# Kernel optimization log

Hardware: AMD Instinct MI355X
Metric: run time of the kernel (lower is better)

The kernel has to match this reference:

```python
import jax, jax.numpy as jnp
import numpy as np

EPS = 1e-5
GROUPS = 32


def group_norm(x, gamma, beta):
    # x: [b, c, h, w]
    b, c, h, w = x.shape
    xg = x.reshape(b, GROUPS, c // GROUPS, h, w)
    mu = jnp.mean(xg, axis=(2, 3, 4), keepdims=True)
    var = jnp.var(xg, axis=(2, 3, 4), keepdims=True)
    xg = (xg - mu) / jnp.sqrt(var + EPS)
    x = xg.reshape(b, c, h, w)
    return x * gamma[None, :, None, None] + beta[None, :, None, None]


def conv1x1(x, w, bias):
    # x: [b, c_in, h, w], w: [c_out, c_in] -> [b, c_out, h, w]
    return jnp.einsum('oc,bchw->bohw', w, x) + bias[None, :, None, None]


def setup_inputs() -> dict:
    key = jax.random.key(0)
    ks = jax.random.split(key, 6)
    c = 512
    s = 1.0 / np.sqrt(c)
    x = jax.random.normal(ks[0], (8, c, 64, 64), dtype=jnp.float32)
    return {
        'x': x,
        'gn_gamma': jnp.ones((c,), jnp.float32),
        'gn_beta': jnp.zeros((c,), jnp.float32),
        'wq': jax.random.normal(ks[1], (c, c), jnp.float32) * s,
        'bq': jnp.zeros((c,), jnp.float32),
        'wk': jax.random.normal(ks[2], (c, c), jnp.float32) * s,
        'bk': jnp.zeros((c,), jnp.float32),
        'wv': jax.random.normal(ks[3], (c, c), jnp.float32) * s,
        'bv': jnp.zeros((c,), jnp.float32),
        'wo': jax.random.normal(ks[4], (c, c), jnp.float32) * s,
        'bo': jnp.zeros((c,), jnp.float32),
    }


def reference(x, gn_gamma, gn_beta, wq, bq, wk, bk, wv, bv, wo, bo):
    b, c, h, w = x.shape
    hidden = group_norm(x, gn_gamma, gn_beta)
    q = conv1x1(hidden, wq, bq).reshape(b, c, h * w).transpose(0, 2, 1)  # [b, hw, c]
    k = conv1x1(hidden, wk, bk).reshape(b, c, h * w)                      # [b, c, hw]
    v = conv1x1(hidden, wv, bv).reshape(b, c, h * w).transpose(0, 2, 1)  # [b, hw, c]
    # NOTE: faithful to source — attention logits are MULTIPLIED by sqrt(c)
    attn = jnp.einsum('bqc,bck->bqk', q, k) * jnp.float32(c) ** 0.5
    attn = jax.nn.softmax(attn, axis=-1)
    attn_h = jnp.einsum('bqk,bkc->bqc', attn, v)                          # [b, hw, c]
    attn_h = attn_h.transpose(0, 2, 1).reshape(b, c, h, w)
    return x + conv1x1(attn_h, wo, bo)
```

## Files before the change

### kernel.cpp

```cpp
#include <hip/hip_runtime.h>
#include <stdint.h>

typedef unsigned short u16;
typedef unsigned int u32;
typedef __attribute__((ext_vector_type(4))) float f32x4;
typedef __attribute__((ext_vector_type(8))) __bf16 bf16x8;
typedef __attribute__((ext_vector_type(4))) unsigned short u16x4;

#define DEVINL __device__ __forceinline__

DEVINL u16 f2bf(float f) {
  u32 u = __builtin_bit_cast(u32, f);
  u32 r = (u + 0x7fffu + ((u >> 16) & 1u)) >> 16;
  return (u16)r;
}
DEVINL float bf2f(u16 h) {
  u32 u = ((u32)h) << 16;
  return __builtin_bit_cast(float, u);
}

DEVINL f32x4 mfma16(bf16x8 a, bf16x8 b, f32x4 c) {
  return __builtin_amdgcn_mfma_f32_16x16x32_bf16(a, b, c, 0, 0, 0);
}

DEVINL void gload_lds16(const void* g, void* l) {
  auto gp = (__attribute__((address_space(1))) void*)(reinterpret_cast<uintptr_t>(g));
  auto lp = (__attribute__((address_space(3))) void*)(u32)(reinterpret_cast<uintptr_t>(l));
  __builtin_amdgcn_global_load_lds(gp, lp, 16, 0, 0);
}

template <int ROWS, int KCS, int NT>
DEVINL void stage_tile(const u16* __restrict__ g, int ld, char* lds, int tid) {
  constexpr int SWZ = (KCS - 1) < 7 ? (KCS - 1) : 7;
  constexpr int CH = ROWS * KCS;
#pragma unroll
  for (int c0 = 0; c0 < CH; c0 += NT) {
    int c = c0 + tid;
    int row = c / KCS;
    int slot = c & (KCS - 1);
    const u16* src = g + (size_t)row * ld + ((slot ^ (row & SWZ)) << 3);
    char* dst = lds + (((size_t)(c0 + (tid & ~63))) << 4);
    gload_lds16(src, dst);
  }
}

template <int KCS, int SWZM>
DEVINL bf16x8 fragk(const char* lds, int row, int kslot) {
  return *reinterpret_cast<const bf16x8*>(
      lds + (size_t)row * (KCS * 16) + (size_t)((kslot ^ (row & SWZM)) << 4));
}

__global__ __launch_bounds__(256) void gn_stats(const float* __restrict__ x,
                                                float* __restrict__ smean,
                                                float* __restrict__ srstd) {
  const int bg = blockIdx.x;
  const float4* base = reinterpret_cast<const float4*>(x + (size_t)bg * 65536);
  float s = 0.f, ss = 0.f;
  for (int i = threadIdx.x; i < 16384; i += 256) {
    float4 v = base[i];
    s += v.x + v.y + v.z + v.w;
    ss += v.x * v.x + v.y * v.y + v.z * v.z + v.w * v.w;
  }
#pragma unroll
  for (int off = 1; off < 64; off <<= 1) {
    s += __shfl_xor(s, off);
    ss += __shfl_xor(ss, off);
  }
  __shared__ float rs_[4], rss_[4];
  int w = threadIdx.x >> 6;
  if ((threadIdx.x & 63) == 0) { rs_[w] = s; rss_[w] = ss; }
  __syncthreads();
  if (threadIdx.x == 0) {
    float S = rs_[0] + rs_[1] + rs_[2] + rs_[3];
    float SS = rss_[0] + rss_[1] + rss_[2] + rss_[3];
    float mu = S * (1.0f / 65536.0f);
    float var = SS * (1.0f / 65536.0f) - mu * mu;
    smean[bg] = mu;
    srstd[bg] = 1.0f / sqrtf(var + 1e-5f);
  }
}

__global__ __launch_bounds__(256) void gn_apply(
    const float* __restrict__ x, const float* __restrict__ gamma,
    const float* __restrict__ beta, const float* __restrict__ smean,
    const float* __restrict__ srstd, u16* __restrict__ hhi, u16* __restrict__ hlo) {
  __shared__ __align__(16) u16 thi[128][136];
  __shared__ __align__(16) u16 tlo[128][136];
  const int b = blockIdx.z, p0 = blockIdx.y * 128, c0 = blockIdx.x * 128;
  const int tid = threadIdx.x;
  const int ci = tid >> 1, ph = tid & 1;
  const int c = c0 + ci;
  const int bg = b * 32 + (c >> 4);
  const float mu = smean[bg], rstd = srstd[bg];
  const float ga = gamma[c] * rstd;
  const float be = beta[c] - mu * ga;
  const float* xrow = x + ((size_t)(b * 512 + c)) * 4096 + p0;
#pragma unroll
  for (int s = 0; s < 16; s++) {
    int pj = ph * 4 + s * 8;
    float4 v = *reinterpret_cast<const float4*>(xrow + pj);
    float h0 = v.x * ga + be, h1 = v.y * ga + be, h2 = v.z * ga + be, h3 = v.w * ga + be;
    u16 a0 = f2bf(h0), a1 = f2bf(h1), a2 = f2bf(h2), a3 = f2bf(h3);
    thi[pj + 0][ci] = a0; tlo[pj + 0][ci] = f2bf(h0 - bf2f(a0));
    thi[pj + 1][ci] = a1; tlo[pj + 1][ci] = f2bf(h1 - bf2f(a1));
    thi[pj + 2][ci] = a2; tlo[pj + 2][ci] = f2bf(h2 - bf2f(a2));
    thi[pj + 3][ci] = a3; tlo[pj + 3][ci] = f2bf(h3 - bf2f(a3));
  }
  __syncthreads();
  u16* oh = hhi + ((size_t)b * 4096 + p0) * 512 + c0;
  u16* ol = hlo + ((size_t)b * 4096 + p0) * 512 + c0;
  for (int cc = tid; cc < 2048; cc += 256) {
    int p = cc >> 4, sli = cc & 15;
    *reinterpret_cast<bf16x8*>(oh + (size_t)p * 512 + sli * 8) =
        *reinterpret_cast<const bf16x8*>(&thi[p][sli * 8]);
    *reinterpret_cast<bf16x8*>(ol + (size_t)p * 512 + sli * 8) =
        *reinterpret_cast<const bf16x8*>(&tlo[p][sli * 8]);
  }
}

__global__ __launch_bounds__(256) void prep_w(
    const float* __restrict__ wq, const float* __restrict__ wk,
    const float* __restrict__ wv, const float* __restrict__ wo,
    u16* __restrict__ wqh, u16* __restrict__ wql, u16* __restrict__ wkh,
    u16* __restrict__ wkl, u16* __restrict__ wvb, u16* __restrict__ wob) {
  int i = blockIdx.x * 256 + threadIdx.x;
  if (i >= 262144) return;
  float a = wq[i]; u16 h = f2bf(a); wqh[i] = h; wql[i] = f2bf(a - bf2f(h));
  float bb = wk[i]; h = f2bf(bb); wkh[i] = h; wkl[i] = f2bf(bb - bf2f(h));
  wvb[i] = f2bf(wv[i]);
  wob[i] = f2bf(wo[i]);
}

template <int MODE>
__global__ __launch_bounds__(256, 2) void conv_gemm(
    const u16* __restrict__ A0, const u16* __restrict__ A1,
    const u16* __restrict__ B0, const u16* __restrict__ B1,
    const float* __restrict__ bias, const float* __restrict__ xres,
    u16* __restrict__ o0, u16* __restrict__ o1, float* __restrict__ of,
    long sAb, long sBb) {
  constexpr int LDSZ = (MODE == 0) ? 65536 : ((MODE == 1) ? 34816 : 32768);
  __shared__ __align__(16) char lds[LDSZ];
  char* ldsA = lds;
  char* ldsB = lds + 16384;

  const int b = blockIdx.z;
  const int n0 = blockIdx.x * 128;
  const int m0 = blockIdx.y * 128;
  const int tid = threadIdx.x;
  const int lane = tid & 63;
  const int w = tid >> 6;
  const int li = lane & 15, gq = lane >> 4;
  const int wm = (w >> 1) * 64, wn = (w & 1) * 64;

  const u16* Ag = A0 + (size_t)b * sAb + (size_t)m0 * 512;
  const u16* Bg = B0 + (size_t)b * sBb + (size_t)n0 * 512;
  const u16* Ag1 = (MODE == 0) ? (A1 + (size_t)b * sAb + (size_t)m0 * 512) : nullptr;
  const u16* Bg1 = (MODE == 0) ? (B1 + (size_t)b * sBb + (size_t)n0 * 512) : nullptr;

  f32x4 acc[4][4] = {};

  for (int k0 = 0; k0 < 512; k0 += 64) {
    __syncthreads();
    stage_tile<128, 8, 256>(Ag + k0, 512, ldsA, tid);
    stage_tile<128, 8, 256>(Bg + k0, 512, ldsB, tid);
    if (MODE == 0) {
      stage_tile<128, 8, 256>(Ag1 + k0, 512, lds + 32768, tid);
      stage_tile<128, 8, 256>(Bg1 + k0, 512, lds + 49152, tid);
    }
    __syncthreads();
#pragma unroll
    for (int kk = 0; kk < 2; kk++) {
      bf16x8 aF[4], bF[4], aL[4], bL[4];
#pragma unroll
      for (int t = 0; t < 4; t++) {
        aF[t] = fragk<8, 7>(ldsA, wm + t * 16 + li, kk * 4 + gq);
        bF[t] = fragk<8, 7>(ldsB, wn + t * 16 + li, kk * 4 + gq);
        if (MODE == 0) {
          aL[t] = fragk<8, 7>(lds + 32768, wm + t * 16 + li, kk * 4 + gq);
          bL[t] = fragk<8, 7>(lds + 49152, wn + t * 16 + li, kk * 4 + gq);
        }
      }
#pragma unroll
      for (int mt = 0; mt < 4; mt++)
#pragma unroll
        for (int nt = 0; nt < 4; nt++) {
          acc[mt][nt] = mfma16(aF[mt], bF[nt], acc[mt][nt]);
          if (MODE == 0) {
            acc[mt][nt] = mfma16(aF[mt], bL[nt], acc[mt][nt]);
            acc[mt][nt] = mfma16(aL[mt], bF[nt], acc[mt][nt]);
          }
        }
    }
  }

  if (MODE == 0) {
#pragma unroll
    for (int nt = 0; nt < 4; nt++) {
      int gn = n0 + wn + nt * 16 + li;
      float bs = bias[gn];
#pragma unroll
      for (int mt = 0; mt < 4; mt++)
#pragma unroll
        for (int r = 0; r < 4; r++) {
          int gm = m0 + wm + mt * 16 + gq * 4 + r;
          float v = acc[mt][nt][r] + bs;
          u16 hi = f2bf(v);
          size_t idx = ((size_t)b * 4096 + gm) * 512 + gn;
          o0[idx] = hi;
          o1[idx] = f2bf(v - bf2f(hi));
        }
    }
  } else if (MODE == 1) {
    __syncthreads();
    u16* vt = (u16*)lds;
#pragma unroll
    for (int nt = 0; nt < 4; nt++) {
      int ol = wn + nt * 16 + li;
      float bs = bias[n0 + ol];
#pragma unroll
      for (int mt = 0; mt < 4; mt++)
#pragma unroll
        for (int r = 0; r < 4; r++) {
          int pl = wm + mt * 16 + gq * 4 + r;
          vt[ol * 136 + pl] = f2bf(acc[mt][nt][r] + bs);
        }
    }
    __syncthreads();
    for (int c = tid; c < 2048; c += 256) {
      int o = c >> 4, sl = c & 15;
      bf16x8 val = *reinterpret_cast<const bf16x8*>(vt + o * 136 + sl * 8);
      *reinterpret_cast<bf16x8*>(o0 + ((size_t)b * 512 + n0 + o) * 4096 + m0 + sl * 8) = val;
    }
  } else {
#pragma unroll
    for (int nt = 0; nt < 4; nt++) {
      int gn = n0 + wn + nt * 16 + li;
#pragma unroll
      for (int mt = 0; mt < 4; mt++)
#pragma unroll
        for (int r = 0; r < 4; r++) {
          int gm = m0 + wm + mt * 16 + gq * 4 + r;
          size_t idx = ((size_t)b * 512 + gm) * 4096 + gn;
          of[idx] = acc[mt][nt][r] + bias[gm] + xres[idx];
        }
    }
  }
}

#define S2C 32.64446259f

__global__ __launch_bounds__(512) void flash_attn(
    const u16* __restrict__ qhi, const u16* __restrict__ qlo,
    const u16* __restrict__ khi, const u16* __restrict__ klo,
    const u16* __restrict__ vbuf, u16* __restrict__ oout) {
  __shared__ __align__(16) char ldsK[65536];
  __shared__ float sm[64], sl[64], srs[64];
  __shared__ float pmax[2][64], psum[2][64];

  const int bid = blockIdx.x;
  const int b = bid & 7, qt = bid >> 3;
  const int i0 = qt * 64;
  const int tid = threadIdx.x;
  const int lane = tid & 63, w = tid >> 6;
  const int li = lane & 15, gq = lane >> 4;
  const int mt_qk = w >> 1, jh = w & 1;
  const int wc = w * 64;

  if (tid < 64) { sm[tid] = -3.0e38f; sl[tid] = 0.0f; }

  const u16* Kh = khi + (size_t)b * 4096 * 512;
  const u16* Kl = klo + (size_t)b * 4096 * 512;
  const u16* qbh = qhi + ((size_t)(b * 4096 + i0 + mt_qk * 16 + li)) * 512 + gq * 8;
  const u16* qbl = qlo + ((size_t)(b * 4096 + i0 + mt_qk * 16 + li)) * 512 + gq * 8;
  const u16* Vb = vbuf + (size_t)b * 512 * 4096;
  u16* Pl = (u16*)(ldsK + 32768);

  stage_tile<128, 8, 512>(Kh, 512, ldsK, tid);
  stage_tile<128, 8, 512>(Kl, 512, ldsK + 16384, tid);

  f32x4 Oa[4][4] = {};

  for (int j0 = 0; j0 < 4096; j0 += 128) {
    f32x4 lg[4] = {};
#pragma unroll
    for (int cc = 0; cc < 8; cc++) {
      const int c0 = cc * 64;
      const char* cur = ldsK + (size_t)(cc & 1) * 32768;
      __syncthreads();
      if (cc < 7) {
        char* nxt = ldsK + (size_t)((cc + 1) & 1) * 32768;
        stage_tile<128, 8, 512>(Kh + (size_t)j0 * 512 + c0 + 64, 512, nxt, tid);
        stage_tile<128, 8, 512>(Kl + (size_t)j0 * 512 + c0 + 64, 512, nxt + 16384, tid);
      }
#pragma unroll
      for (int kk = 0; kk < 2; kk++) {
        bf16x8 qhf = *reinterpret_cast<const bf16x8*>(qbh + c0 + kk * 32);
        bf16x8 qlf = *reinterpret_cast<const bf16x8*>(qbl + c0 + kk * 32);
        __builtin_amdgcn_s_setprio(1);
#pragma unroll
        for (int nt = 0; nt < 4; nt++) {
          int krow = jh * 64 + nt * 16 + li;
          bf16x8 bh = fragk<8, 7>(cur, krow, kk * 4 + gq);
          bf16x8 bl = fragk<8, 7>(cur + 16384, krow, kk * 4 + gq);
          lg[nt] = mfma16(bh, qhf, lg[nt]);
          lg[nt] = mfma16(bl, qhf, lg[nt]);
          lg[nt] = mfma16(bh, qlf, lg[nt]);
        }
        __builtin_amdgcn_s_setprio(0);
      }
    }
    bf16x8 vA[4], vB[4];
#pragma unroll
    for (int t = 0; t < 4; t++)
      vA[t] = *reinterpret_cast<const bf16x8*>(
          Vb + (size_t)(wc + t * 16 + li) * 4096 + j0 + gq * 8);
#pragma unroll
    for (int t = 0; t < 4; t++)
      vB[t] = *reinterpret_cast<const bf16x8*>(
          Vb + (size_t)(wc + t * 16 + li) * 4096 + j0 + 32 + gq * 8);
    const int i_ = mt_qk * 16 + li;
    {
      float mx = lg[0][0];
#pragma unroll
      for (int nt = 0; nt < 4; nt++)
#pragma unroll
        for (int r = 0; r < 4; r++) mx = fmaxf(mx, lg[nt][r]);
      mx = fmaxf(mx, __shfl_xor(mx, 16));
      mx = fmaxf(mx, __shfl_xor(mx, 32));
      if (lane < 16) pmax[jh][i_] = mx;
    }
    __syncthreads();
    if (tid < 64) {
      float tm = fmaxf(pmax[0][tid], pmax[1][tid]);
      float mo = sm[tid];
      float mn = fmaxf(mo, tm);
      float rs = exp2f(S2C * (mo - mn));
      sm[tid] = mn; srs[tid] = rs; sl[tid] *= rs;
    }
    __syncthreads();
    {
      float mn = sm[i_];
      float ps = 0.0f;
#pragma unroll
      for (int nt = 0; nt < 4; nt++) {
        float p0 = exp2f(S2C * (lg[nt][0] - mn));
        float p1 = exp2f(S2C * (lg[nt][1] - mn));
        float p2 = exp2f(S2C * (lg[nt][2] - mn));
        float p3 = exp2f(S2C * (lg[nt][3] - mn));
        ps += (p0 + p1) + (p2 + p3);
        u16x4 pk = {f2bf(p0), f2bf(p1), f2bf(p2), f2bf(p3)};
        int jb = jh * 64 + nt * 16 + gq * 4;
        char* dst = (char*)Pl + (size_t)i_ * 256 +
                    (((jb >> 3) ^ (i_ & 15)) << 4) + ((jb << 1) & 15);
        *reinterpret_cast<u16x4*>(dst) = pk;
      }
      ps += __shfl_xor(ps, 16);
      ps += __shfl_xor(ps, 32);
      if (lane < 16) psum[jh][i_] = ps;
    }
    __syncthreads();
    if (tid < 64) sl[tid] += psum[0][tid] + psum[1][tid];
    if (j0 + 128 < 4096) {
      stage_tile<128, 8, 512>(Kh + (size_t)(j0 + 128) * 512, 512, ldsK, tid);
      stage_tile<128, 8, 512>(Kl + (size_t)(j0 + 128) * 512, 512, ldsK + 16384, tid);
    }
#pragma unroll
    for (int mt = 0; mt < 4; mt++)
#pragma unroll
      for (int r = 0; r < 4; r++) {
        float rr = srs[mt * 16 + gq * 4 + r];
#pragma unroll
        for (int nt = 0; nt < 4; nt++) Oa[mt][nt][r] *= rr;
      }
#define PVSTEP(JJ, VREG)                                                      \
    {                                                                         \
      __builtin_amdgcn_s_setprio(1);                                          \
      _Pragma("unroll")                                                       \
      for (int mt = 0; mt < 4; mt++) {                                        \
        bf16x8 pa = fragk<16, 15>((const char*)Pl, mt * 16 + li, (JJ) * 4 + gq); \
        _Pragma("unroll")                                                     \
        for (int nt = 0; nt < 4; nt++)                                        \
          Oa[mt][nt] = mfma16(pa, VREG[nt], Oa[mt][nt]);                      \
      }                                                                       \
      __builtin_amdgcn_s_setprio(0);                                          \
    }
    PVSTEP(0, vA)
#pragma unroll
    for (int t = 0; t < 4; t++)
      vA[t] = *reinterpret_cast<const bf16x8*>(
          Vb + (size_t)(wc + t * 16 + li) * 4096 + j0 + 64 + gq * 8);
    PVSTEP(1, vB)
#pragma unroll
    for (int t = 0; t < 4; t++)
      vB[t] = *reinterpret_cast<const bf16x8*>(
          Vb + (size_t)(wc + t * 16 + li) * 4096 + j0 + 96 + gq * 8);
    PVSTEP(2, vA)
    PVSTEP(3, vB)
#undef PVSTEP
  }

  __syncthreads();
#pragma unroll
  for (int mt = 0; mt < 4; mt++)
#pragma unroll
    for (int r = 0; r < 4; r++) {
      int i2 = mt * 16 + gq * 4 + r;
      float inv = 1.0f / sl[i2];
#pragma unroll
      for (int nt = 0; nt < 4; nt++) {
        float o = Oa[mt][nt][r] * inv;
        oout[((size_t)(b * 4096 + i0 + i2)) * 512 + wc + nt * 16 + li] = f2bf(o);
      }
    }
}

extern "C" void kernel_launch(void* const* d_in, const int* in_sizes, int n_in,
                              void* d_out, int out_size, void* d_ws, size_t ws_size,
                              hipStream_t stream) {
  const float* x = (const float*)d_in[0];
  const float* gamma = (const float*)d_in[1];
  const float* beta = (const float*)d_in[2];
  const float* wq = (const float*)d_in[3];
  const float* bq = (const float*)d_in[4];
  const float* wk = (const float*)d_in[5];
  const float* bk = (const float*)d_in[6];
  const float* wv = (const float*)d_in[7];
  const float* bv = (const float*)d_in[8];
  const float* wo = (const float*)d_in[9];
  const float* bo = (const float*)d_in[10];

  char* ws = (char*)d_ws;
  const size_t SZ = (size_t)8 * 4096 * 512 * 2;
  const size_t NEED = 7 * SZ + 6 * (size_t)524288 + 2048;
  if (ws_size < NEED) return;

  u16* hhi = (u16*)(ws);
  u16* hlo = (u16*)(ws + SZ);
  u16* qhi = (u16*)(ws + 2 * SZ);
  u16* qlo = (u16*)(ws + 3 * SZ);
  u16* khi = (u16*)(ws + 4 * SZ);
  u16* klo = (u16*)(ws + 5 * SZ);
  u16* vbf = (u16*)(ws + 6 * SZ);
  u16* ah  = qhi;
  u16* wqh = (u16*)(ws + 7 * SZ);
  u16* wql = wqh + 262144;
  u16* wkh = wql + 262144;
  u16* wkl = wkh + 262144;
  u16* wvb = wkl + 262144;
  u16* wob = wvb + 262144;
  float* smean = (float*)(wob + 262144);
  float* srstd = smean + 256;

  prep_w<<<1024, 256, 0, stream>>>(wq, wk, wv, wo, wqh, wql, wkh, wkl, wvb, wob);
  gn_stats<<<256, 256, 0, stream>>>(x, smean, srstd);
  gn_apply<<<dim3(4, 32, 8), 256, 0, stream>>>(x, gamma, beta, smean, srstd, hhi, hlo);
  conv_gemm<0><<<dim3(4, 32, 8), 256, 0, stream>>>(hhi, hlo, wqh, wql, bq, nullptr,
                                                   qhi, qlo, nullptr, (long)4096 * 512, 0);
  conv_gemm<0><<<dim3(4, 32, 8), 256, 0, stream>>>(hhi, hlo, wkh, wkl, bk, nullptr,
                                                   khi, klo, nullptr, (long)4096 * 512, 0);
  conv_gemm<1><<<dim3(4, 32, 8), 256, 0, stream>>>(hhi, nullptr, wvb, nullptr, bv, nullptr,
                                                   vbf, nullptr, nullptr, (long)4096 * 512, 0);
  flash_attn<<<512, 512, 0, stream>>>(qhi, qlo, khi, klo, vbf, ah);
  conv_gemm<2><<<dim3(32, 4, 8), 256, 0, stream>>>(wob, nullptr, ah, nullptr, bo, x,
                                                   nullptr, nullptr, (float*)d_out,
                                                   0, (long)4096 * 512);
}
```

Before: 1.235 ms.

## Enlarge flash attention query tile to 128 rows with per-warp softmax state

Each block now handles 128 query rows instead of 64, and each warp owns 16 full query rows across all 128 keys. Online-softmax max and sum therefore stay in registers, which removes the cross-warp pmax/psum exchange and two barriers per key tile. The next K tile's first chunk is now prefetched inside the last channel step rather than after softmax. The cost is twice the accumulator registers (Oa 8x4, lg 8), a separate P buffer in LDS, and only 256 blocks, which risks lower occupancy or register spills.

```diff
diff --git a/kernel.cpp b/kernel.cpp
--- a/kernel.cpp
+++ b/kernel.cpp
@@ -254,43 +254,45 @@
     const u16* __restrict__ khi, const u16* __restrict__ klo,
     const u16* __restrict__ vbuf, u16* __restrict__ oout) {
   __shared__ __align__(16) char ldsK[65536];
-  __shared__ float sm[64], sl[64], srs[64];
-  __shared__ float pmax[2][64], psum[2][64];
+  __shared__ __align__(16) char ldsP[32768];
+  __shared__ float srs_l[128];
+  __shared__ float sl_l[128];
 
   const int bid = blockIdx.x;
   const int b = bid & 7, qt = bid >> 3;
-  const int i0 = qt * 64;
+  const int i0 = qt * 128;
   const int tid = threadIdx.x;
   const int lane = tid & 63, w = tid >> 6;
   const int li = lane & 15, gq = lane >> 4;
-  const int mt_qk = w >> 1, jh = w & 1;
   const int wc = w * 64;
-
-  if (tid < 64) { sm[tid] = -3.0e38f; sl[tid] = 0.0f; }
 
   const u16* Kh = khi + (size_t)b * 4096 * 512;
   const u16* Kl = klo + (size_t)b * 4096 * 512;
-  const u16* qbh = qhi + ((size_t)(b * 4096 + i0 + mt_qk * 16 + li)) * 512 + gq * 8;
-  const u16* qbl = qlo + ((size_t)(b * 4096 + i0 + mt_qk * 16 + li)) * 512 + gq * 8;
+  const u16* qbh = qhi + ((size_t)(b * 4096 + i0 + w * 16 + li)) * 512 + gq * 8;
+  const u16* qbl = qlo + ((size_t)(b * 4096 + i0 + w * 16 + li)) * 512 + gq * 8;
   const u16* Vb = vbuf + (size_t)b * 512 * 4096;
-  u16* Pl = (u16*)(ldsK + 32768);
 
   stage_tile<128, 8, 512>(Kh, 512, ldsK, tid);
   stage_tile<128, 8, 512>(Kl, 512, ldsK + 16384, tid);
 
-  f32x4 Oa[4][4] = {};
+  float m_run = -3.0e38f, l_run = 0.0f;
+  f32x4 Oa[8][4] = {};
 
   for (int j0 = 0; j0 < 4096; j0 += 128) {
-    f32x4 lg[4] = {};
+    f32x4 lg[8] = {};
 #pragma unroll
     for (int cc = 0; cc < 8; cc++) {
       const int c0 = cc * 64;
       const char* cur = ldsK + (size_t)(cc & 1) * 32768;
       __syncthreads();
-      if (cc < 7) {
+      {
         char* nxt = ldsK + (size_t)((cc + 1) & 1) * 32768;
-        stage_tile<128, 8, 512>(Kh + (size_t)j0 * 512 + c0 + 64, 512, nxt, tid);
-        stage_tile<128, 8, 512>(Kl + (size_t)j0 * 512 + c0 + 64, 512, nxt + 16384, tid);
+        int nj0 = (cc < 7) ? j0 : j0 + 128;
+        int nc0 = (cc < 7) ? c0 + 64 : 0;
+        if (nj0 < 4096) {
+          stage_tile<128, 8, 512>(Kh + (size_t)nj0 * 512 + nc0, 512, nxt, tid);
+          stage_tile<128, 8, 512>(Kl + (size_t)nj0 * 512 + nc0, 512, nxt + 16384, tid);
+        }
       }
 #pragma unroll
       for (int kk = 0; kk < 2; kk++) {
@@ -298,10 +300,9 @@
         bf16x8 qlf = *reinterpret_cast<const bf16x8*>(qbl + c0 + kk * 32);
         __builtin_amdgcn_s_setprio(1);
 #pragma unroll
-        for (int nt = 0; nt < 4; nt++) {
-          int krow = jh * 64 + nt * 16 + li;
-          bf16x8 bh = fragk<8, 7>(cur, krow, kk * 4 + gq);
-          bf16x8 bl = fragk<8, 7>(cur + 16384, krow, kk * 4 + gq);
+        for (int nt = 0; nt < 8; nt++) {
+          bf16x8 bh = fragk<8, 7>(cur, nt * 16 + li, kk * 4 + gq);
+          bf16x8 bl = fragk<8, 7>(cur + 16384, nt * 16 + li, kk * 4 + gq);
           lg[nt] = mfma16(bh, qhf, lg[nt]);
           lg[nt] = mfma16(bl, qhf, lg[nt]);
           lg[nt] = mfma16(bh, qlf, lg[nt]);
@@ -318,66 +319,52 @@
     for (int t = 0; t < 4; t++)
       vB[t] = *reinterpret_cast<const bf16x8*>(
           Vb + (size_t)(wc + t * 16 + li) * 4096 + j0 + 32 + gq * 8);
-    const int i_ = mt_qk * 16 + li;
     {
       float mx = lg[0][0];
 #pragma unroll
-      for (int nt = 0; nt < 4; nt++)
+      for (int nt = 0; nt < 8; nt++)
 #pragma unroll
         for (int r = 0; r < 4; r++) mx = fmaxf(mx, lg[nt][r]);
       mx = fmaxf(mx, __shfl_xor(mx, 16));
       mx = fmaxf(mx, __shfl_xor(mx, 32));
-      if (lane < 16) pmax[jh][i_] = mx;
-    }
-    __syncthreads();
-    if (tid < 64) {
-      float tm = fmaxf(pmax[0][tid], pmax[1][tid]);
-      float mo = sm[tid];
-      float mn = fmaxf(mo, tm);
-      float rs = exp2f(S2C * (mo - mn));
-      sm[tid] = mn; srs[tid] = rs; sl[tid] *= rs;
-    }
-    __syncthreads();
-    {
-      float mn = sm[i_];
+      float mn = fmaxf(m_run, mx);
+      float rs = exp2f(S2C * (m_run - mn));
+      m_run = mn;
+      l_run *= rs;
       float ps = 0.0f;
-#pragma unroll
-      for (int nt = 0; nt < 4; nt++) {
+      const int i_ = w * 16 + li;
+#pragma unroll
+      for (int nt = 0; nt < 8; nt++) {
         float p0 = exp2f(S2C * (lg[nt][0] - mn));
         float p1 = exp2f(S2C * (lg[nt][1] - mn));
         float p2 = exp2f(S2C * (lg[nt][2] - mn));
         float p3 = exp2f(S2C * (lg[nt][3] - mn));
         ps += (p0 + p1) + (p2 + p3);
         u16x4 pk = {f2bf(p0), f2bf(p1), f2bf(p2), f2bf(p3)};
-        int jb = jh * 64 + nt * 16 + gq * 4;
-        char* dst = (char*)Pl + (size_t)i_ * 256 +
-                    (((jb >> 3) ^ (i_ & 15)) << 4) + ((jb << 1) & 15);
+        int jb = nt * 16 + gq * 4;
+        char* dst = ldsP + (size_t)i_ * 256 + (((jb >> 3) ^ li) << 4) + ((jb << 1) & 15);
         *reinterpret_cast<u16x4*>(dst) = pk;
       }
       ps += __shfl_xor(ps, 16);
       ps += __shfl_xor(ps, 32);
-      if (lane < 16) psum[jh][i_] = ps;
+      l_run += ps;
+      if (gq == 0) srs_l[i_] = rs;
     }
     __syncthreads();
-    if (tid < 64) sl[tid] += psum[0][tid] + psum[1][tid];
-    if (j0 + 128 < 4096) {
-      stage_tile<128, 8, 512>(Kh + (size_t)(j0 + 128) * 512, 512, ldsK, tid);
-      stage_tile<128, 8, 512>(Kl + (size_t)(j0 + 128) * 512, 512, ldsK + 16384, tid);
-    }
-#pragma unroll
-    for (int mt = 0; mt < 4; mt++)
-#pragma unroll
-      for (int r = 0; r < 4; r++) {
-        float rr = srs[mt * 16 + gq * 4 + r];
-#pragma unroll
-        for (int nt = 0; nt < 4; nt++) Oa[mt][nt][r] *= rr;
-      }
+#pragma unroll
+    for (int mt = 0; mt < 8; mt++) {
+      f32x4 rr = *reinterpret_cast<const f32x4*>(&srs_l[mt * 16 + gq * 4]);
+#pragma unroll
+      for (int nt = 0; nt < 4; nt++)
+#pragma unroll
+        for (int r = 0; r < 4; r++) Oa[mt][nt][r] *= rr[r];
+    }
 #define PVSTEP(JJ, VREG)                                                      \
     {                                                                         \
       __builtin_amdgcn_s_setprio(1);                                          \
       _Pragma("unroll")                                                       \
-      for (int mt = 0; mt < 4; mt++) {                                        \
-        bf16x8 pa = fragk<16, 15>((const char*)Pl, mt * 16 + li, (JJ) * 4 + gq); \
+      for (int mt = 0; mt < 8; mt++) {                                        \
+        bf16x8 pa = fragk<16, 15>(ldsP, mt * 16 + li, (JJ) * 4 + gq);         \
         _Pragma("unroll")                                                     \
         for (int nt = 0; nt < 4; nt++)                                        \
           Oa[mt][nt] = mfma16(pa, VREG[nt], Oa[mt][nt]);                      \
@@ -399,19 +386,22 @@
 #undef PVSTEP
   }
 
+  if (gq == 0) sl_l[w * 16 + li] = l_run;
   __syncthreads();
 #pragma unroll
-  for (int mt = 0; mt < 4; mt++)
+  for (int mt = 0; mt < 8; mt++) {
+    f32x4 l4 = *reinterpret_cast<const f32x4*>(&sl_l[mt * 16 + gq * 4]);
 #pragma unroll
     for (int r = 0; r < 4; r++) {
       int i2 = mt * 16 + gq * 4 + r;
-      float inv = 1.0f / sl[i2];
+      float inv = 1.0f / l4[r];
 #pragma unroll
       for (int nt = 0; nt < 4; nt++) {
         float o = Oa[mt][nt][r] * inv;
         oout[((size_t)(b * 4096 + i0 + i2)) * 512 + wc + nt * 16 + li] = f2bf(o);
       }
     }
+  }
 }
 
 extern "C" void kernel_launch(void* const* d_in, const int* in_sizes, int n_in,
@@ -460,7 +450,7 @@
                                                    khi, klo, nullptr, (long)4096 * 512, 0);
   conv_gemm<1><<<dim3(4, 32, 8), 256, 0, stream>>>(hhi, nullptr, wvb, nullptr, bv, nullptr,
                                                    vbf, nullptr, nullptr, (long)4096 * 512, 0);
-  flash_attn<<<512, 512, 0, stream>>>(qhi, qlo, khi, klo, vbf, ah);
+  flash_attn<<<256, 512, 0, stream>>>(qhi, qlo, khi, klo, vbf, ah);
   conv_gemm<2><<<dim3(32, 4, 8), 256, 0, stream>>>(wob, nullptr, ah, nullptr, bo, x,
                                                    nullptr, nullptr, (float*)d_out,
                                                    0, (long)4096 * 512);
```

Result: slower. 1.402 ms (+13.5%).

## Deepen K-tile pipeline to four LDS stages with prefetch-distance two and partial waits

Applied to the files above, without the earlier changes.

The K staging ring in flash attention grows from two to four 32KB LDS buffers, and loads are issued two chunks ahead, continuing across j0 iterations. This replaces the separate restage that used to happen after the softmax. Full __syncthreads are replaced by barriers that wait only on vmcnt(8) or lgkmcnt(0), so later global loads can stay in flight. Q fragments are prefetched into registers one chunk ahead, and P moves to its own LDS buffer. The cost is about 144KB of LDS per block and reliance on exact vmcnt accounting, where a wrong count could let compute read K data that has not yet arrived.

```diff
diff --git a/kernel.cpp b/kernel.cpp
--- a/kernel.cpp
+++ b/kernel.cpp
@@ -49,6 +49,19 @@
   return *reinterpret_cast<const bf16x8*>(
       lds + (size_t)row * (KCS * 16) + (size_t)((kslot ^ (row & SWZM)) << 4));
 }
+
+#define KBAR()                                               \
+  do {                                                       \
+    asm volatile("s_waitcnt vmcnt(8)" ::: "memory");         \
+    __builtin_amdgcn_s_barrier();                            \
+    __builtin_amdgcn_sched_barrier(0);                       \
+  } while (0)
+#define LBAR()                                               \
+  do {                                                       \
+    asm volatile("s_waitcnt lgkmcnt(0)" ::: "memory");       \
+    __builtin_amdgcn_s_barrier();                            \
+    __builtin_amdgcn_sched_barrier(0);                       \
+  } while (0)
 
 __global__ __launch_bounds__(256) void gn_stats(const float* __restrict__ x,
                                                 float* __restrict__ smean,
@@ -253,7 +266,8 @@
     const u16* __restrict__ qhi, const u16* __restrict__ qlo,
     const u16* __restrict__ khi, const u16* __restrict__ klo,
     const u16* __restrict__ vbuf, u16* __restrict__ oout) {
-  __shared__ __align__(16) char ldsK[65536];
+  __shared__ __align__(16) char ldsK[131072];
+  __shared__ __align__(16) char ldsP[16384];
   __shared__ float sm[64], sl[64], srs[64];
   __shared__ float pmax[2][64], psum[2][64];
 
@@ -273,10 +287,16 @@
   const u16* qbh = qhi + ((size_t)(b * 4096 + i0 + mt_qk * 16 + li)) * 512 + gq * 8;
   const u16* qbl = qlo + ((size_t)(b * 4096 + i0 + mt_qk * 16 + li)) * 512 + gq * 8;
   const u16* Vb = vbuf + (size_t)b * 512 * 4096;
-  u16* Pl = (u16*)(ldsK + 32768);
+  u16* Pl = (u16*)ldsP;
 
   stage_tile<128, 8, 512>(Kh, 512, ldsK, tid);
   stage_tile<128, 8, 512>(Kl, 512, ldsK + 16384, tid);
+  stage_tile<128, 8, 512>(Kh + 64, 512, ldsK + 32768, tid);
+  stage_tile<128, 8, 512>(Kl + 64, 512, ldsK + 32768 + 16384, tid);
+  bf16x8 qh0 = *reinterpret_cast<const bf16x8*>(qbh);
+  bf16x8 qh1 = *reinterpret_cast<const bf16x8*>(qbh + 32);
+  bf16x8 ql0 = *reinterpret_cast<const bf16x8*>(qbl);
+  bf16x8 ql1 = *reinterpret_cast<const bf16x8*>(qbl + 32);
 
   f32x4 Oa[4][4] = {};
 
@@ -284,29 +304,39 @@
     f32x4 lg[4] = {};
 #pragma unroll
     for (int cc = 0; cc < 8; cc++) {
-      const int c0 = cc * 64;
-      const char* cur = ldsK + (size_t)(cc & 1) * 32768;
-      __syncthreads();
-      if (cc < 7) {
-        char* nxt = ldsK + (size_t)((cc + 1) & 1) * 32768;
-        stage_tile<128, 8, 512>(Kh + (size_t)j0 * 512 + c0 + 64, 512, nxt, tid);
-        stage_tile<128, 8, 512>(Kl + (size_t)j0 * 512 + c0 + 64, 512, nxt + 16384, tid);
+      const char* cur = ldsK + (size_t)(cc & 3) * 32768;
+      KBAR();
+      {
+        char* nxt = ldsK + (size_t)((cc + 2) & 3) * 32768;
+        const int nj0 = (cc < 6) ? j0 : j0 + 128;
+        if (nj0 < 4096) {
+          const int nc0 = ((cc + 2) & 7) * 64;
+          stage_tile<128, 8, 512>(Kh + (size_t)nj0 * 512 + nc0, 512, nxt, tid);
+          stage_tile<128, 8, 512>(Kl + (size_t)nj0 * 512 + nc0, 512, nxt + 16384, tid);
+        }
       }
 #pragma unroll
       for (int kk = 0; kk < 2; kk++) {
-        bf16x8 qhf = *reinterpret_cast<const bf16x8*>(qbh + c0 + kk * 32);
-        bf16x8 qlf = *reinterpret_cast<const bf16x8*>(qbl + c0 + kk * 32);
+        bf16x8 qh_ = kk ? qh1 : qh0;
+        bf16x8 ql_ = kk ? ql1 : ql0;
         __builtin_amdgcn_s_setprio(1);
 #pragma unroll
         for (int nt = 0; nt < 4; nt++) {
           int krow = jh * 64 + nt * 16 + li;
           bf16x8 bh = fragk<8, 7>(cur, krow, kk * 4 + gq);
           bf16x8 bl = fragk<8, 7>(cur + 16384, krow, kk * 4 + gq);
-          lg[nt] = mfma16(bh, qhf, lg[nt]);
-          lg[nt] = mfma16(bl, qhf, lg[nt]);
-          lg[nt] = mfma16(bh, qlf, lg[nt]);
+          lg[nt] = mfma16(bh, qh_, lg[nt]);
+          lg[nt] = mfma16(bl, qh_, lg[nt]);
+          lg[nt] = mfma16(bh, ql_, lg[nt]);
         }
         __builtin_amdgcn_s_setprio(0);
+      }
+      {
+        const int nq = ((cc + 1) & 7) * 64;
+        qh0 = *reinterpret_cast<const bf16x8*>(qbh + nq);
+        qh1 = *reinterpret_cast<const bf16x8*>(qbh + nq + 32);
+        ql0 = *reinterpret_cast<const bf16x8*>(qbl + nq);
+        ql1 = *reinterpret_cast<const bf16x8*>(qbl + nq + 32);
       }
     }
     bf16x8 vA[4], vB[4];
@@ -329,7 +359,7 @@
       mx = fmaxf(mx, __shfl_xor(mx, 32));
       if (lane < 16) pmax[jh][i_] = mx;
     }
-    __syncthreads();
+    LBAR();
     if (tid < 64) {
       float tm = fmaxf(pmax[0][tid], pmax[1][tid]);
       float mo = sm[tid];
@@ -337,7 +367,7 @@
       float rs = exp2f(S2C * (mo - mn));
       sm[tid] = mn; srs[tid] = rs; sl[tid] *= rs;
     }
-    __syncthreads();
+    LBAR();
     {
       float mn = sm[i_];
       float ps = 0.0f;
@@ -358,12 +388,8 @@
       ps += __shfl_xor(ps, 32);
       if (lane < 16) psum[jh][i_] = ps;
     }
-    __syncthreads();
+    LBAR();
     if (tid < 64) sl[tid] += psum[0][tid] + psum[1][tid];
-    if (j0 + 128 < 4096) {
-      stage_tile<128, 8, 512>(Kh + (size_t)(j0 + 128) * 512, 512, ldsK, tid);
-      stage_tile<128, 8, 512>(Kl + (size_t)(j0 + 128) * 512, 512, ldsK + 16384, tid);
-    }
 #pragma unroll
     for (int mt = 0; mt < 4; mt++)
 #pragma unroll
```

Measured after the change: 1.327 ms. 1.07x slower.

## Share staged K tiles across two query groups in 1024-thread attention blocks

Applied to the files above, without the earlier changes.

The flash attention kernel now processes 128 query rows per block using 1024 threads, split into two 64-row groups. Both groups share the same double-buffered K hi/lo tiles in LDS, and each group keeps its own P scratch region. This halves the grid to 256 blocks and cuts K staging and global K reads per query row, so each loaded K tile feeds twice the MFMA work. In exchange, every block-wide barrier now spans 16 waves, and the 1024-thread launch bound limits per-thread registers, which risks spills given the large accumulator state.

```diff
diff --git a/kernel.cpp b/kernel.cpp
--- a/kernel.cpp
+++ b/kernel.cpp
@@ -249,34 +249,37 @@
 
 #define S2C 32.64446259f
 
-__global__ __launch_bounds__(512) void flash_attn(
+__global__ __launch_bounds__(1024, 1) void flash_attn(
     const u16* __restrict__ qhi, const u16* __restrict__ qlo,
     const u16* __restrict__ khi, const u16* __restrict__ klo,
     const u16* __restrict__ vbuf, u16* __restrict__ oout) {
   __shared__ __align__(16) char ldsK[65536];
-  __shared__ float sm[64], sl[64], srs[64];
-  __shared__ float pmax[2][64], psum[2][64];
+  __shared__ float sm[128], sl[128], srs[128];
+  __shared__ float pmax[2][128], psum[2][128];
 
   const int bid = blockIdx.x;
   const int b = bid & 7, qt = bid >> 3;
-  const int i0 = qt * 64;
+  const int i0 = qt * 128;
   const int tid = threadIdx.x;
   const int lane = tid & 63, w = tid >> 6;
+  const int g = w >> 3, w8 = w & 7;
   const int li = lane & 15, gq = lane >> 4;
-  const int mt_qk = w >> 1, jh = w & 1;
-  const int wc = w * 64;
-
-  if (tid < 64) { sm[tid] = -3.0e38f; sl[tid] = 0.0f; }
+  const int mt_qk = w8 >> 1, jh = w8 & 1;
+  const int wc = w8 * 64;
+
+  if (tid < 128) { sm[tid] = -3.0e38f; sl[tid] = 0.0f; }
 
   const u16* Kh = khi + (size_t)b * 4096 * 512;
   const u16* Kl = klo + (size_t)b * 4096 * 512;
-  const u16* qbh = qhi + ((size_t)(b * 4096 + i0 + mt_qk * 16 + li)) * 512 + gq * 8;
-  const u16* qbl = qlo + ((size_t)(b * 4096 + i0 + mt_qk * 16 + li)) * 512 + gq * 8;
+  const u16* qbh =
+      qhi + ((size_t)(b * 4096 + i0 + g * 64 + mt_qk * 16 + li)) * 512 + gq * 8;
+  const u16* qbl =
+      qlo + ((size_t)(b * 4096 + i0 + g * 64 + mt_qk * 16 + li)) * 512 + gq * 8;
   const u16* Vb = vbuf + (size_t)b * 512 * 4096;
-  u16* Pl = (u16*)(ldsK + 32768);
-
-  stage_tile<128, 8, 512>(Kh, 512, ldsK, tid);
-  stage_tile<128, 8, 512>(Kl, 512, ldsK + 16384, tid);
+  u16* Pl = (u16*)(ldsK + 32768 + g * 16384);
+
+  stage_tile<128, 8, 1024>(Kh, 512, ldsK, tid);
+  stage_tile<128, 8, 1024>(Kl, 512, ldsK + 16384, tid);
 
   f32x4 Oa[4][4] = {};
 
@@ -289,8 +292,8 @@
       __syncthreads();
       if (cc < 7) {
         char* nxt = ldsK + (size_t)((cc + 1) & 1) * 32768;
-        stage_tile<128, 8, 512>(Kh + (size_t)j0 * 512 + c0 + 64, 512, nxt, tid);
-        stage_tile<128, 8, 512>(Kl + (size_t)j0 * 512 + c0 + 64, 512, nxt + 16384, tid);
+        stage_tile<128, 8, 1024>(Kh + (size_t)j0 * 512 + c0 + 64, 512, nxt, tid);
+        stage_tile<128, 8, 1024>(Kl + (size_t)j0 * 512 + c0 + 64, 512, nxt + 16384, tid);
       }
 #pragma unroll
       for (int kk = 0; kk < 2; kk++) {
@@ -318,7 +321,8 @@
     for (int t = 0; t < 4; t++)
       vB[t] = *reinterpret_cast<const bf16x8*>(
           Vb + (size_t)(wc + t * 16 + li) * 4096 + j0 + 32 + gq * 8);
-    const int i_ = mt_qk * 16 + li;
+    const int il = mt_qk * 16 + li;
+    const int i_ = g * 64 + il;
     {
       float mx = lg[0][0];
 #pragma unroll
@@ -330,7 +334,7 @@
       if (lane < 16) pmax[jh][i_] = mx;
     }
     __syncthreads();
-    if (tid < 64) {
+    if (tid < 128) {
       float tm = fmaxf(pmax[0][tid], pmax[1][tid]);
       float mo = sm[tid];
       float mn = fmaxf(mo, tm);
@@ -350,8 +354,8 @@
         ps += (p0 + p1) + (p2 + p3);
         u16x4 pk = {f2bf(p0), f2bf(p1), f2bf(p2), f2bf(p3)};
         int jb = jh * 64 + nt * 16 + gq * 4;
-        char* dst = (char*)Pl + (size_t)i_ * 256 +
-                    (((jb >> 3) ^ (i_ & 15)) << 4) + ((jb << 1) & 15);
+        char* dst = (char*)Pl + (size_t)il * 256 +
+                    (((jb >> 3) ^ (il & 15)) << 4) + ((jb << 1) & 15);
         *reinterpret_cast<u16x4*>(dst) = pk;
       }
       ps += __shfl_xor(ps, 16);
@@ -359,16 +363,16 @@
       if (lane < 16) psum[jh][i_] = ps;
     }
     __syncthreads();
-    if (tid < 64) sl[tid] += psum[0][tid] + psum[1][tid];
+    if (tid < 128) sl[tid] += psum[0][tid] + psum[1][tid];
     if (j0 + 128 < 4096) {
-      stage_tile<128, 8, 512>(Kh + (size_t)(j0 + 128) * 512, 512, ldsK, tid);
-      stage_tile<128, 8, 512>(Kl + (size_t)(j0 + 128) * 512, 512, ldsK + 16384, tid);
+      stage_tile<128, 8, 1024>(Kh + (size_t)(j0 + 128) * 512, 512, ldsK, tid);
+      stage_tile<128, 8, 1024>(Kl + (size_t)(j0 + 128) * 512, 512, ldsK + 16384, tid);
     }
 #pragma unroll
     for (int mt = 0; mt < 4; mt++)
 #pragma unroll
       for (int r = 0; r < 4; r++) {
-        float rr = srs[mt * 16 + gq * 4 + r];
+        float rr = srs[g * 64 + mt * 16 + gq * 4 + r];
 #pragma unroll
         for (int nt = 0; nt < 4; nt++) Oa[mt][nt][r] *= rr;
       }
@@ -404,12 +408,13 @@
   for (int mt = 0; mt < 4; mt++)
 #pragma unroll
     for (int r = 0; r < 4; r++) {
-      int i2 = mt * 16 + gq * 4 + r;
-      float inv = 1.0f / sl[i2];
+      int il2 = mt * 16 + gq * 4 + r;
+      float inv = 1.0f / sl[g * 64 + il2];
 #pragma unroll
       for (int nt = 0; nt < 4; nt++) {
         float o = Oa[mt][nt][r] * inv;
-        oout[((size_t)(b * 4096 + i0 + i2)) * 512 + wc + nt * 16 + li] = f2bf(o);
+        oout[((size_t)(b * 4096 + i0 + g * 64 + il2)) * 512 + wc + nt * 16 + li] =
+            f2bf(o);
       }
     }
 }
@@ -460,7 +465,7 @@
                                                    khi, klo, nullptr, (long)4096 * 512, 0);
   conv_gemm<1><<<dim3(4, 32, 8), 256, 0, stream>>>(hhi, nullptr, wvb, nullptr, bv, nullptr,
                                                    vbf, nullptr, nullptr, (long)4096 * 512, 0);
-  flash_attn<<<512, 512, 0, stream>>>(qhi, qlo, khi, klo, vbf, ah);
+  flash_attn<<<256, 1024, 0, stream>>>(qhi, qlo, khi, klo, vbf, ah);
   conv_gemm<2><<<dim3(32, 4, 8), 256, 0, stream>>>(wob, nullptr, ah, nullptr, bo, x,
                                                    nullptr, nullptr, (float*)d_out,
                                                    0, (long)4096 * 512);
```

Result: slower. 1.806 ms (+46.3%).
